# Kernel tuning notes

Hardware: AMD Instinct MI355X
Metric: run time of the kernel (lower is better)

## Reference

```python
import jax, jax.numpy as jnp
import numpy as np
from jax import lax

B, C, H, W, K, R = 8, 64, 128, 128, 3, 4  # batch, channels, height, width, kernel_size, region_number


def _leaky(x):
    return jnp.where(x >= 0, x, 0.1 * x)


def _asign_index(kernel, guide):
    # kernel: (b,R,c,h,w), guide: (b,R,h,w) -> hard top-1 region routing -> (b,c,h,w)
    mask = jax.nn.one_hot(jnp.argmax(guide, axis=1), R, axis=1, dtype=kernel.dtype)  # (b,R,h,w)
    return jnp.sum(kernel * mask[:, :, None], axis=1)


def _conv2d(x, w, pad):
    return lax.conv_general_dilated(x, w, (1, 1), [(pad, pad), (pad, pad)],
                                    dimension_numbers=('NCHW', 'OIHW', 'NCHW'))


def setup_inputs() -> dict:
    key = jax.random.key(0)
    ks = jax.random.split(key, 12)
    s = 0.05
    return {
        'x0': jax.random.normal(ks[0], (B, C, H, W), jnp.float32),
        'deg': jax.random.normal(ks[1], (B, C), jnp.float32),
        'q_map': jax.random.normal(ks[2], (B, 1, H, W), jnp.float32),
        'w_k1': jax.random.normal(ks[3], (C, C), jnp.float32) * s,
        'w_k2': jax.random.normal(ks[4], (R, C * K * K, C // R), jnp.float32) * s,
        'w_conv': jax.random.normal(ks[5], (C, C), jnp.float32) * s,
        'b_conv': jax.random.normal(ks[6], (C,), jnp.float32) * s,
        'w_ca1': jax.random.normal(ks[7], (C, C), jnp.float32) * s,
        'w_ca2': jax.random.normal(ks[8], (R, C, C // R), jnp.float32) * s,
        'w_g1': jax.random.normal(ks[9], (R, 1, K, K), jnp.float32) * s,
        'b_g1': jnp.zeros((R,), jnp.float32),
        'w_g2': jax.random.normal(ks[10], (R, 1, K, K), jnp.float32) * s,
        'b_g2': jnp.zeros((R,), jnp.float32),
    }


def reference(x0, deg, q_map, w_k1, w_k2, w_conv, b_conv, w_ca1, w_ca2, w_g1, b_g1, w_g2, b_g2):
    b, c, h, w = x0.shape
    pad = (K - 1) // 2
    # --- dynamic per-sample, per-channel depthwise kernels from degradation rep ---
    y = _leaky(deg @ w_k1.T)                                             # 1x1 conv1d -> (b, c)
    kflat = jnp.einsum('bgi,goi->bgo', y.reshape(b, R, c // R), w_k2)    # grouped 1x1 conv1d
    kernel = kflat.reshape(b, R, c, K, K).transpose(0, 2, 1, 3, 4)       # (b,c,R,K,K)
    rhs = kernel.reshape(b * c * R, 1, K, K)
    out = lax.conv_general_dilated(x0.reshape(1, b * c, h, w), rhs, (1, 1),
                                   [(pad, pad), (pad, pad)],
                                   dimension_numbers=('NCHW', 'OIHW', 'NCHW'),
                                   feature_group_count=b * c)            # (1, b*c*R, h, w)
    out = _leaky(out).reshape(b, c, R, h, w).transpose(0, 2, 1, 3, 4)    # (b,R,c,h,w)
    g1 = _conv2d(q_map, w_g1, 1) + b_g1[None, :, None, None]             # (b,R,h,w)
    out = _asign_index(out, g1)                                          # (b,c,h,w)
    out = jnp.einsum('bchw,oc->bohw', out, w_conv) + b_conv[None, :, None, None]
    # --- channel-attention (CA_layer) branch ---
    a = _leaky(deg @ w_ca1.T)                                            # (b, c)
    att = jax.nn.sigmoid(jnp.einsum('bgi,goi->bgo', a.reshape(b, R, c // R), w_ca2))  # (b,R,c)
    out2 = x0[:, None] * att[:, :, :, None, None]                        # (b,R,c,h,w)
    g2 = _conv2d(q_map, w_g2, 1) + b_g2[None, :, None, None]
    out2 = _asign_index(out2, g2)
    return out + out2
```

## Files before the change

### kernel.cpp

```cpp
#include <hip/hip_runtime.h>
#include <hip/hip_bf16.h>
#include <math.h>

#define Bn 8
#define Cn 64
#define Hn 128
#define Wn 128
#define Rn 4

typedef __bf16 v8bf __attribute__((ext_vector_type(8)));
typedef float  v16f __attribute__((ext_vector_type(16)));

__device__ __forceinline__ float leaky(float x) { return x >= 0.f ? x : 0.1f * x; }

__device__ __forceinline__ unsigned bf16pair(float a, float b) {
    __hip_bfloat16 ha = __float2bfloat16(a);
    __hip_bfloat16 hb = __float2bfloat16(b);
    return (unsigned)*reinterpret_cast<unsigned short*>(&ha) |
           ((unsigned)*reinterpret_cast<unsigned short*>(&hb) << 16);
}

__global__ __launch_bounds__(256) void precomp_kernel(
    const float* __restrict__ deg, const float* __restrict__ w_k1,
    const float* __restrict__ w_k2, const float* __restrict__ w_ca1,
    const float* __restrict__ w_ca2, const float* __restrict__ w_conv,
    float* __restrict__ kern_g, float* __restrict__ att_g,
    unsigned short* __restrict__ wbf)
{
    const int tid = threadIdx.x;
    if (blockIdx.x == Bn) {
        for (int f = tid; f < Cn * Cn; f += 256) {
            __hip_bfloat16 hx = __float2bfloat16(w_conv[f]);
            wbf[f] = *reinterpret_cast<unsigned short*>(&hx);
        }
        return;
    }
    const int b = blockIdx.x;
    __shared__ float y_s[64], a_s[64];
    if (tid < 64) {
        float sy = 0.f, sa = 0.f;
#pragma unroll 8
        for (int j = 0; j < 64; ++j) {
            float d = deg[b * 64 + j];
            sy += d * w_k1[tid * 64 + j];
            sa += d * w_ca1[tid * 64 + j];
        }
        y_s[tid] = leaky(sy);
        a_s[tid] = leaky(sa);
    }
    __syncthreads();
    for (int f = tid; f < Cn * Rn * 9; f += 256) {
        int c = f / 36;
        int j = f - c * 36;
        int r = j / 9;
        int kk = j - r * 9;
        int o = c * 9 + kk;
        const float* wp = &w_k2[(r * 576 + o) * 16];
        const float* yp = &y_s[r * 16];
        float s = 0.f;
#pragma unroll
        for (int i = 0; i < 16; ++i) s += yp[i] * wp[i];
        kern_g[b * 2304 + f] = s;
    }
    {
        int r = tid >> 6, o = tid & 63;
        const float* wp = &w_ca2[(r * 64 + o) * 16];
        const float* ap = &a_s[r * 16];
        float s = 0.f;
#pragma unroll
        for (int i = 0; i < 16; ++i) s += ap[i] * wp[i];
        att_g[b * 256 + tid] = 1.f / (1.f + expf(-s));
    }
}

__global__ __launch_bounds__(512) void da_main(
    const float* __restrict__ x0, const float* __restrict__ q_map,
    const unsigned short* __restrict__ wbf, const float* __restrict__ b_conv,
    const float* __restrict__ w_g1, const float* __restrict__ b_g1,
    const float* __restrict__ w_g2, const float* __restrict__ b_g2,
    const float* __restrict__ kern_g, const float* __restrict__ att_g,
    float* __restrict__ out)
{
    __shared__ __align__(16) float kern_lds[Cn * 48];
    __shared__ __align__(16) unsigned short wc_lds[8][Cn][8];
    __shared__ __align__(16) unsigned short t_lds[Wn * Cn];
    __shared__ float att_lds[Rn * 68];
    __shared__ float bias_lds[Cn];
    __shared__ unsigned ridx[Wn];

    const int tid = threadIdx.x;
    const int ob = blockIdx.x;
    const int sb = ((ob & 7) << 7) | (ob >> 3);
    const int b = sb >> 7;
    const int h = sb & 127;

    const int lane = tid & 63;
    const int w = tid & 127;
    const int q = tid >> 7;

    for (int f = tid; f < Cn * Rn * 9; f += 512) {
        int c = f / 36;
        int j = f - c * 36;
        int r = j / 9;
        int kk = j - r * 9;
        kern_lds[c * 48 + r * 12 + kk] = kern_g[b * 2304 + f];
    }
    {
        int cq = tid & 7, o = tid >> 3;
        *(v8bf*)&wc_lds[cq][o][0] = *(const v8bf*)&wbf[o * 64 + cq * 8];
    }
    if (tid < 256) att_lds[(tid >> 6) * 68 + (tid & 63)] = att_g[b * 256 + tid];
    if (tid < 64) bias_lds[tid] = b_conv[tid];

    if (tid < 128) {
        const int wc = tid;
        float qv[9];
#pragma unroll
        for (int dh = 0; dh < 3; ++dh) {
            int row = h - 1 + dh;
#pragma unroll
            for (int dw = 0; dw < 3; ++dw) {
                int col = wc - 1 + dw;
                qv[dh * 3 + dw] = (row >= 0 && row < Hn && col >= 0 && col < Wn)
                                      ? q_map[(b * Hn + row) * Wn + col] : 0.f;
            }
        }
        float best1 = -1e30f, best2 = -1e30f;
        int r1 = 0, r2 = 0;
#pragma unroll
        for (int r = 0; r < Rn; ++r) {
            float s1 = b_g1[r], s2 = b_g2[r];
#pragma unroll
            for (int k = 0; k < 9; ++k) {
                s1 += qv[k] * w_g1[r * 9 + k];
                s2 += qv[k] * w_g2[r * 9 + k];
            }
            if (s1 > best1) { best1 = s1; r1 = r; }
            if (s2 > best2) { best2 = s2; r2 = r; }
        }
        ridx[wc] = (unsigned)r1 | ((unsigned)r2 << 16);
    }
    __syncthreads();

    const bool okm = (h > 0);
    const bool okp = (h < Hn - 1);
    const float* xbase = x0 + (size_t)(b * Cn) * Hn * Wn + h * Wn + w;
    const int swz = (w & 7) << 4;
    const int r1 = (int)(ridx[w] & 0xffffu);
    const int eoff = (lane == 0) ? ((w == 0) ? 0 : -1)
                   : (lane == 63) ? ((w == 127) ? 0 : 1) : 0;
    const bool eok = !((lane == 0 && w == 0) || (lane == 63 && w == 127));

    float nvm[2], nv0[2], nvp[2], nem[2], ne0[2], nep[2];

#define LOADP(P)                                                          \
    do {                                                                  \
        _Pragma("unroll")                                                 \
        for (int u = 0; u < 2; ++u) {                                     \
            const float* xc = xbase + (16 * q + 2 * (P) + u) * (Hn * Wn); \
            nvm[u] = okm ? xc[-Wn] : 0.f;                                 \
            nv0[u] = xc[0];                                               \
            nvp[u] = okp ? xc[Wn] : 0.f;                                  \
            const float* xe = xc + eoff;                                  \
            nem[u] = okm ? xe[-Wn] : 0.f;                                 \
            ne0[u] = xe[0];                                               \
            nep[u] = okp ? xe[Wn] : 0.f;                                  \
        }                                                                 \
    } while (0)

    LOADP(0);
#pragma unroll
    for (int p = 0; p < 8; ++p) {
        float avm[2] = {nvm[0], nvm[1]}, av0[2] = {nv0[0], nv0[1]},
              avp[2] = {nvp[0], nvp[1]};
        float aem[2] = {nem[0], nem[1]}, ae0[2] = {ne0[0], ne0[1]},
              aep[2] = {nep[0], nep[1]};
        if (p < 7) LOADP(p + 1);

        float tt[2];
#pragma unroll
        for (int u = 0; u < 2; ++u) {
            const int c = 16 * q + 2 * p + u;
            float vm = avm[u], v0 = av0[u], vp = avp[u];
            float lm = __shfl_up(vm, 1), l0 = __shfl_up(v0, 1), lp = __shfl_up(vp, 1);
            float rm = __shfl_down(vm, 1), r0 = __shfl_down(v0, 1), rp = __shfl_down(vp, 1);
            float em = eok ? aem[u] : 0.f;
            float e0 = eok ? ae0[u] : 0.f;
            float ep = eok ? aep[u] : 0.f;
            if (lane == 0)  { lm = em; l0 = e0; lp = ep; }
            if (lane == 63) { rm = em; r0 = e0; rp = ep; }
            const float* kp = &kern_lds[c * 48 + r1 * 12];
            float4 k03 = *(const float4*)kp;
            float4 k47 = *(const float4*)(kp + 4);
            float k8 = kp[8];
            float t = lm * k03.x + vm * k03.y + rm * k03.z
                    + l0 * k03.w + v0 * k47.x + r0 * k47.y
                    + lp * k47.z + vp * k47.w + rp * k8;
            tt[u] = leaky(t);
        }
        unsigned pk = bf16pair(tt[0], tt[1]);
        int cbyte = (16 * q + 2 * p) * 2;
        *(unsigned*)((char*)t_lds + w * 128 + (cbyte ^ swz)) = pk;
    }
#undef LOADP
    __syncthreads();

    const int v = tid >> 6;
    const int wt = v & 3;
    const int oh = v >> 2;
    const int col = lane & 31;
    const int kh = lane >> 5;
    const int wn = wt * 32 + col;

    v8bf Bf[4];
#pragma unroll
    for (int ks = 0; ks < 4; ++ks) {
        int cbyte = (16 * ks + 8 * kh) * 2;
        Bf[ks] = *(const v8bf*)((const char*)t_lds + wn * 128 + (cbyte ^ ((wn & 7) << 4)));
    }

    v16f acc;
#pragma unroll
    for (int i = 0; i < 16; ++i) acc[i] = 0.f;

#pragma unroll
    for (int ks = 0; ks < 4; ++ks) {
        const int cq = 2 * ks + kh;
        v8bf Af = *(const v8bf*)&wc_lds[cq][oh * 32 + col][0];
        acc = __builtin_amdgcn_mfma_f32_32x32x16_bf16(Af, Bf[ks], acc, 0, 0, 0);
    }

    const int r2e = (int)(ridx[wn] >> 16);
    const float* xcol = x0 + ((size_t)(b * Cn + oh * 32) * Hn + h) * Wn + wn;
    float* ocol = out + ((size_t)(b * Cn + oh * 32) * Hn + h) * Wn + wn;

#pragma unroll
    for (int r = 0; r < 16; ++r) {
        int row = (r & 3) + 8 * (r >> 2) + 4 * kh;
        int o = oh * 32 + row;
        float xv = xcol[(size_t)row * (Hn * Wn)];
        float res = acc[r] + bias_lds[o] + xv * att_lds[r2e * 68 + o];
        ocol[(size_t)row * (Hn * Wn)] = res;
    }
}

extern "C" void kernel_launch(void* const* d_in, const int* in_sizes, int n_in,
                              void* d_out, int out_size, void* d_ws, size_t ws_size,
                              hipStream_t stream)
{
    const float* x0     = (const float*)d_in[0];
    const float* deg    = (const float*)d_in[1];
    const float* q_map  = (const float*)d_in[2];
    const float* w_k1   = (const float*)d_in[3];
    const float* w_k2   = (const float*)d_in[4];
    const float* w_conv = (const float*)d_in[5];
    const float* b_conv = (const float*)d_in[6];
    const float* w_ca1  = (const float*)d_in[7];
    const float* w_ca2  = (const float*)d_in[8];
    const float* w_g1   = (const float*)d_in[9];
    const float* b_g1   = (const float*)d_in[10];
    const float* w_g2   = (const float*)d_in[11];
    const float* b_g2   = (const float*)d_in[12];
    float* outp   = (float*)d_out;
    float* kern_g = (float*)d_ws;
    float* att_g  = kern_g + Bn * Cn * Rn * 9;
    unsigned short* wbf = (unsigned short*)(att_g + Bn * 256);

    precomp_kernel<<<Bn + 1, 256, 0, stream>>>(deg, w_k1, w_k2, w_ca1, w_ca2,
                                               w_conv, kern_g, att_g, wbf);
    da_main<<<Bn * Hn, 512, 0, stream>>>(x0, q_map, wbf, b_conv,
                                         w_g1, b_g1, w_g2, b_g2,
                                         kern_g, att_g, outp);
}
```

Baseline: 36.14 us.

## Double-depth prefetch of x0 across sync and pack bf16 tile into 16-byte LDS stores

Moves the first __syncthreads after issuing two stages of x0 global loads, so the loads overlap the guide/routing setup, and deepens the prefetch to two channel pairs ahead. The intermediate LDS tile changes from a swizzled row-major layout to a [chunk][w][8] layout, so each thread writes 16-byte vectors instead of 4-byte stores and the MFMA B-fragment reads need no swizzle. The cost is more registers held for the deeper prefetch, which may lower occupancy.

```diff
diff --git a/kernel.cpp b/kernel.cpp
--- a/kernel.cpp
+++ b/kernel.cpp
@@ -83,7 +83,7 @@
 {
     __shared__ __align__(16) float kern_lds[Cn * 48];
     __shared__ __align__(16) unsigned short wc_lds[8][Cn][8];
-    __shared__ __align__(16) unsigned short t_lds[Wn * Cn];
+    __shared__ __align__(16) unsigned short t_lds[8][Wn][8];
     __shared__ float att_lds[Rn * 68];
     __shared__ float bias_lds[Cn];
     __shared__ unsigned ridx[Wn];
@@ -140,42 +140,49 @@
         }
         ridx[wc] = (unsigned)r1 | ((unsigned)r2 << 16);
     }
-    __syncthreads();
 
     const bool okm = (h > 0);
     const bool okp = (h < Hn - 1);
     const float* xbase = x0 + (size_t)(b * Cn) * Hn * Wn + h * Wn + w;
-    const int swz = (w & 7) << 4;
-    const int r1 = (int)(ridx[w] & 0xffffu);
     const int eoff = (lane == 0) ? ((w == 0) ? 0 : -1)
                    : (lane == 63) ? ((w == 127) ? 0 : 1) : 0;
     const bool eok = !((lane == 0 && w == 0) || (lane == 63 && w == 127));
 
-    float nvm[2], nv0[2], nvp[2], nem[2], ne0[2], nep[2];
-
-#define LOADP(P)                                                          \
+    float pvm[2][2], pv0[2][2], pvp[2][2], pem[2][2], pe0[2][2], pep[2][2];
+
+#define LOADP(P, B)                                                       \
     do {                                                                  \
         _Pragma("unroll")                                                 \
         for (int u = 0; u < 2; ++u) {                                     \
             const float* xc = xbase + (16 * q + 2 * (P) + u) * (Hn * Wn); \
-            nvm[u] = okm ? xc[-Wn] : 0.f;                                 \
-            nv0[u] = xc[0];                                               \
-            nvp[u] = okp ? xc[Wn] : 0.f;                                  \
+            pvm[B][u] = okm ? xc[-Wn] : 0.f;                              \
+            pv0[B][u] = xc[0];                                            \
+            pvp[B][u] = okp ? xc[Wn] : 0.f;                               \
             const float* xe = xc + eoff;                                  \
-            nem[u] = okm ? xe[-Wn] : 0.f;                                 \
-            ne0[u] = xe[0];                                               \
-            nep[u] = okp ? xe[Wn] : 0.f;                                  \
+            pem[B][u] = okm ? xe[-Wn] : 0.f;                              \
+            pe0[B][u] = xe[0];                                            \
+            pep[B][u] = okp ? xe[Wn] : 0.f;                               \
         }                                                                 \
     } while (0)
 
-    LOADP(0);
+    LOADP(0, 0);
+    LOADP(1, 1);
+
+    __syncthreads();
+
+    const int r1 = (int)(ridx[w] & 0xffffu);
+    uint4 pk;
+
 #pragma unroll
     for (int p = 0; p < 8; ++p) {
-        float avm[2] = {nvm[0], nvm[1]}, av0[2] = {nv0[0], nv0[1]},
-              avp[2] = {nvp[0], nvp[1]};
-        float aem[2] = {nem[0], nem[1]}, ae0[2] = {ne0[0], ne0[1]},
-              aep[2] = {nep[0], nep[1]};
-        if (p < 7) LOADP(p + 1);
+        const int B = p & 1;
+        float avm[2] = {pvm[B][0], pvm[B][1]};
+        float av0[2] = {pv0[B][0], pv0[B][1]};
+        float avp[2] = {pvp[B][0], pvp[B][1]};
+        float aem[2] = {pem[B][0], pem[B][1]};
+        float ae0[2] = {pe0[B][0], pe0[B][1]};
+        float aep[2] = {pep[B][0], pep[B][1]};
+        if (p < 6) LOADP(p + 2, B);
 
         float tt[2];
 #pragma unroll
@@ -198,9 +205,15 @@
                     + lp * k47.z + vp * k47.w + rp * k8;
             tt[u] = leaky(t);
         }
-        unsigned pk = bf16pair(tt[0], tt[1]);
-        int cbyte = (16 * q + 2 * p) * 2;
-        *(unsigned*)((char*)t_lds + w * 128 + (cbyte ^ swz)) = pk;
+        unsigned qq = bf16pair(tt[0], tt[1]);
+        if (p == 0) pk.x = qq;
+        else if (p == 1) pk.y = qq;
+        else if (p == 2) pk.z = qq;
+        else if (p == 3) { pk.w = qq; *(uint4*)&t_lds[2 * q][w][0] = pk; }
+        else if (p == 4) pk.x = qq;
+        else if (p == 5) pk.y = qq;
+        else if (p == 6) pk.z = qq;
+        else             { pk.w = qq; *(uint4*)&t_lds[2 * q + 1][w][0] = pk; }
     }
 #undef LOADP
     __syncthreads();
@@ -214,10 +227,8 @@
 
     v8bf Bf[4];
 #pragma unroll
-    for (int ks = 0; ks < 4; ++ks) {
-        int cbyte = (16 * ks + 8 * kh) * 2;
-        Bf[ks] = *(const v8bf*)((const char*)t_lds + wn * 128 + (cbyte ^ ((wn & 7) << 4)));
-    }
+    for (int ks = 0; ks < 4; ++ks)
+        Bf[ks] = *(const v8bf*)&t_lds[2 * ks + kh][wn][0];
 
     v16f acc;
 #pragma unroll
```

Result: slower. 46.01 us (+27.3%).

## Compute column partial sums before shuffling to cut depthwise-conv shuffles

Applied to the files above, without the earlier changes.

The depthwise 3x3 conv now computes per-column partial dot products (left, middle, right) of each lane's own vertical triple and shuffles only the two partials, replacing six shuffles with two per channel. Each neighbour uses its own region's kernel weights. The precomputed kernel is stored column-major and padded to the LDS layout so the main kernel copies it linearly without index math. The cost is four float4 LDS reads per channel instead of about two and a half, more FMAs, and edge lanes now compute a separate partial.

```diff
diff --git a/kernel.cpp b/kernel.cpp
--- a/kernel.cpp
+++ b/kernel.cpp
@@ -60,7 +60,8 @@
         float s = 0.f;
 #pragma unroll
         for (int i = 0; i < 16; ++i) s += yp[i] * wp[i];
-        kern_g[b * 2304 + f] = s;
+        int row = kk / 3, col = kk - row * 3;
+        kern_g[b * 3072 + c * 48 + r * 12 + col * 4 + row] = s;
     }
     {
         int r = tid >> 6, o = tid & 63;
@@ -98,13 +99,8 @@
     const int w = tid & 127;
     const int q = tid >> 7;
 
-    for (int f = tid; f < Cn * Rn * 9; f += 512) {
-        int c = f / 36;
-        int j = f - c * 36;
-        int r = j / 9;
-        int kk = j - r * 9;
-        kern_lds[c * 48 + r * 12 + kk] = kern_g[b * 2304 + f];
-    }
+    for (int f = tid; f < Cn * 48; f += 512)
+        kern_lds[f] = kern_g[b * 3072 + f];
     {
         int cq = tid & 7, o = tid >> 3;
         *(v8bf*)&wc_lds[cq][o][0] = *(const v8bf*)&wbf[o * 64 + cq * 8];
@@ -146,7 +142,13 @@
     const bool okp = (h < Hn - 1);
     const float* xbase = x0 + (size_t)(b * Cn) * Hn * Wn + h * Wn + w;
     const int swz = (w & 7) << 4;
-    const int r1 = (int)(ridx[w] & 0xffffu);
+    const int r1  = (int)(ridx[w] & 0xffffu);
+    const int r1L = (int)(ridx[(w == 0) ? 0 : (w - 1)] & 0xffffu);
+    const int r1R = (int)(ridx[(w == 127) ? 127 : (w + 1)] & 0xffffu);
+    const int offM = r1 * 12 + 4;
+    const int offL = r1R * 12 + 0;
+    const int offR = r1L * 12 + 8;
+    const int offE = r1 * 12 + ((lane == 0) ? 0 : 8);
     const int eoff = (lane == 0) ? ((w == 0) ? 0 : -1)
                    : (lane == 63) ? ((w == 127) ? 0 : 1) : 0;
     const bool eok = !((lane == 0 && w == 0) || (lane == 63 && w == 127));
@@ -181,22 +183,22 @@
 #pragma unroll
         for (int u = 0; u < 2; ++u) {
             const int c = 16 * q + 2 * p + u;
+            const float* kc = &kern_lds[c * 48];
+            float4 kM = *(const float4*)(kc + offM);
+            float4 kL = *(const float4*)(kc + offL);
+            float4 kR = *(const float4*)(kc + offR);
+            float4 kE = *(const float4*)(kc + offE);
             float vm = avm[u], v0 = av0[u], vp = avp[u];
-            float lm = __shfl_up(vm, 1), l0 = __shfl_up(v0, 1), lp = __shfl_up(vp, 1);
-            float rm = __shfl_down(vm, 1), r0 = __shfl_down(v0, 1), rp = __shfl_down(vp, 1);
-            float em = eok ? aem[u] : 0.f;
-            float e0 = eok ? ae0[u] : 0.f;
-            float ep = eok ? aep[u] : 0.f;
-            if (lane == 0)  { lm = em; l0 = e0; lp = ep; }
-            if (lane == 63) { rm = em; r0 = e0; rp = ep; }
-            const float* kp = &kern_lds[c * 48 + r1 * 12];
-            float4 k03 = *(const float4*)kp;
-            float4 k47 = *(const float4*)(kp + 4);
-            float k8 = kp[8];
-            float t = lm * k03.x + vm * k03.y + rm * k03.z
-                    + l0 * k03.w + v0 * k47.x + r0 * k47.y
-                    + lp * k47.z + vp * k47.w + rp * k8;
-            tt[u] = leaky(t);
+            float L = vm * kL.x + v0 * kL.y + vp * kL.z;
+            float M = vm * kM.x + v0 * kM.y + vp * kM.z;
+            float R = vm * kR.x + v0 * kR.y + vp * kR.z;
+            float E = aem[u] * kE.x + ae0[u] * kE.y + aep[u] * kE.z;
+            E = eok ? E : 0.f;
+            float lin = __shfl_up(L, 1);
+            float rin = __shfl_down(R, 1);
+            if (lane == 0)  lin = E;
+            if (lane == 63) rin = E;
+            tt[u] = leaky(lin + M + rin);
         }
         unsigned pk = bf16pair(tt[0], tt[1]);
         int cbyte = (16 * q + 2 * p) * 2;
@@ -263,7 +265,7 @@
     const float* b_g2   = (const float*)d_in[12];
     float* outp   = (float*)d_out;
     float* kern_g = (float*)d_ws;
-    float* att_g  = kern_g + Bn * Cn * Rn * 9;
+    float* att_g  = kern_g + Bn * 3072;
     unsigned short* wbf = (unsigned short*)(att_g + Bn * 256);
 
     precomp_kernel<<<Bn + 1, 256, 0, stream>>>(deg, w_k1, w_k2, w_ca1, w_ca2,
```

After: 36.62 us. No clear change (+1.3%).

## Pre-pad kernel table globally, pack t_lds writes as uint4, overlap loads with barrier

Applied to the files above, without the earlier changes.

The precompute kernel now writes the per-sample depthwise kernels directly in the padded 48-float-per-channel layout, so the main kernel copies them into LDS with a plain linear loop instead of per-element div/mod remapping. The intermediate LDS tile is changed from a swizzled row-major layout to a [channel-octet][w][8] layout, letting each thread accumulate four bf16 pairs in registers and store them as one 16-byte write instead of eight 4-byte writes. The first barrier is moved after the first batch of global x0 loads so those loads can be in flight during the barrier. The new layout drops the XOR swizzle, which may change LDS bank-conflict behaviour on the MFMA operand reads.

```diff
diff --git a/kernel.cpp b/kernel.cpp
--- a/kernel.cpp
+++ b/kernel.cpp
@@ -60,7 +60,7 @@
         float s = 0.f;
 #pragma unroll
         for (int i = 0; i < 16; ++i) s += yp[i] * wp[i];
-        kern_g[b * 2304 + f] = s;
+        kern_g[b * 3072 + c * 48 + r * 12 + kk] = s;
     }
     {
         int r = tid >> 6, o = tid & 63;
@@ -83,7 +83,7 @@
 {
     __shared__ __align__(16) float kern_lds[Cn * 48];
     __shared__ __align__(16) unsigned short wc_lds[8][Cn][8];
-    __shared__ __align__(16) unsigned short t_lds[Wn * Cn];
+    __shared__ __align__(16) unsigned short t_lds[8][Wn][8];
     __shared__ float att_lds[Rn * 68];
     __shared__ float bias_lds[Cn];
     __shared__ unsigned ridx[Wn];
@@ -98,13 +98,8 @@
     const int w = tid & 127;
     const int q = tid >> 7;
 
-    for (int f = tid; f < Cn * Rn * 9; f += 512) {
-        int c = f / 36;
-        int j = f - c * 36;
-        int r = j / 9;
-        int kk = j - r * 9;
-        kern_lds[c * 48 + r * 12 + kk] = kern_g[b * 2304 + f];
-    }
+    for (int f = tid; f < Cn * 48; f += 512)
+        kern_lds[f] = kern_g[b * 3072 + f];
     {
         int cq = tid & 7, o = tid >> 3;
         *(v8bf*)&wc_lds[cq][o][0] = *(const v8bf*)&wbf[o * 64 + cq * 8];
@@ -140,13 +135,10 @@
         }
         ridx[wc] = (unsigned)r1 | ((unsigned)r2 << 16);
     }
-    __syncthreads();
 
     const bool okm = (h > 0);
     const bool okp = (h < Hn - 1);
     const float* xbase = x0 + (size_t)(b * Cn) * Hn * Wn + h * Wn + w;
-    const int swz = (w & 7) << 4;
-    const int r1 = (int)(ridx[w] & 0xffffu);
     const int eoff = (lane == 0) ? ((w == 0) ? 0 : -1)
                    : (lane == 63) ? ((w == 127) ? 0 : 1) : 0;
     const bool eok = !((lane == 0 && w == 0) || (lane == 63 && w == 127));
@@ -169,6 +161,12 @@
     } while (0)
 
     LOADP(0);
+
+    __syncthreads();
+
+    const int r1 = (int)(ridx[w] & 0xffffu);
+    uint4 pk;
+
 #pragma unroll
     for (int p = 0; p < 8; ++p) {
         float avm[2] = {nvm[0], nvm[1]}, av0[2] = {nv0[0], nv0[1]},
@@ -198,9 +196,15 @@
                     + lp * k47.z + vp * k47.w + rp * k8;
             tt[u] = leaky(t);
         }
-        unsigned pk = bf16pair(tt[0], tt[1]);
-        int cbyte = (16 * q + 2 * p) * 2;
-        *(unsigned*)((char*)t_lds + w * 128 + (cbyte ^ swz)) = pk;
+        unsigned qq = bf16pair(tt[0], tt[1]);
+        if (p == 0) pk.x = qq;
+        else if (p == 1) pk.y = qq;
+        else if (p == 2) pk.z = qq;
+        else if (p == 3) { pk.w = qq; *(uint4*)&t_lds[2 * q][w][0] = pk; }
+        else if (p == 4) pk.x = qq;
+        else if (p == 5) pk.y = qq;
+        else if (p == 6) pk.z = qq;
+        else             { pk.w = qq; *(uint4*)&t_lds[2 * q + 1][w][0] = pk; }
     }
 #undef LOADP
     __syncthreads();
@@ -214,10 +218,8 @@
 
     v8bf Bf[4];
 #pragma unroll
-    for (int ks = 0; ks < 4; ++ks) {
-        int cbyte = (16 * ks + 8 * kh) * 2;
-        Bf[ks] = *(const v8bf*)((const char*)t_lds + wn * 128 + (cbyte ^ ((wn & 7) << 4)));
-    }
+    for (int ks = 0; ks < 4; ++ks)
+        Bf[ks] = *(const v8bf*)&t_lds[2 * ks + kh][wn][0];
 
     v16f acc;
 #pragma unroll
@@ -263,7 +265,7 @@
     const float* b_g2   = (const float*)d_in[12];
     float* outp   = (float*)d_out;
     float* kern_g = (float*)d_ws;
-    float* att_g  = kern_g + Bn * Cn * Rn * 9;
+    float* att_g  = kern_g + Bn * 3072;
     unsigned short* wbf = (unsigned short*)(att_g + Bn * 256);
 
     precomp_kernel<<<Bn + 1, 256, 0, stream>>>(deg, w_k1, w_k2, w_ca1, w_ca2,
```

New measurement: 47.47 us. +31.4%, slower.
